# Performance work log

Hardware: AMD Instinct MI355X
Metric: run time of the kernel (lower is better)

## Reference

```python
import jax
import jax.numpy as jnp
from jax import lax
import numpy as np

EMBED_DIM = 768
NUM_HEADS = 12
BATCH = 8
SEQ = 1024
EPS = 1e-07
QK_QBIT = 8
QK_KBIT = 8
AV_ABIT = 8
AV_VBIT = 8
PROJ_WBIT = 8
PROJ_XBIT = 8
SCALE = EMBED_DIM ** (-0.5)  # module uses embed_dim, not head_dim


def _ste(hard, soft):
    # straight-through estimator: forward = hard, backward grad = d(soft)
    return soft + lax.stop_gradient(hard - soft)


def fake_quant_signed(x, bit):
    # _quantize_signed_matrix_train: sign/abs, global-max scaling, STE clamp + round
    sign = lax.stop_gradient(jnp.sign(x))
    a = jnp.abs(x)
    scaling = lax.stop_gradient(jnp.max(a)) + EPS
    y = a / scaling
    y = _ste(jnp.clip(y, 0.0, 1.0), y)          # Clamp.apply (STE)
    levels = 2.0 ** (bit - 1.0) - 1.0
    y = _ste(jnp.round(y * levels) / levels, y)  # Round.apply (STE)
    return y * scaling * sign


def fake_quant_unsigned(x, bit):
    # _quantize_unsigned_matrix_train
    scaling = lax.stop_gradient(jnp.max(x)) + EPS
    y = x / scaling
    y = _ste(jnp.clip(y, 0.0, 1.0), y)
    levels = 2.0 ** bit - 1.0
    y = _ste(jnp.round(y * levels) / levels, y)
    return y * scaling


def asim_linear(x, w, b, wbit, xbit):
    # ASiMLinear in 'Train' mode with signed_act=True: fake-quantize activation
    # and weight, dense matmul, trim_noise=0 -> no perturbation.
    xq = fake_quant_signed(x, xbit)
    wq = fake_quant_signed(w, wbit)
    return jnp.einsum('bnc,oc->bno', xq, wq) + b


def setup_inputs() -> dict:
    key = jax.random.key(0)
    k_x, k_qw, k_qb, k_pw, k_pb = jax.random.split(key, 5)
    x = jax.random.normal(k_x, (BATCH, SEQ, EMBED_DIM), dtype=jnp.float32)
    s = 1.0 / np.sqrt(EMBED_DIM)
    qkv_w = jax.random.normal(k_qw, (3 * EMBED_DIM, EMBED_DIM), dtype=jnp.float32) * s
    qkv_b = jax.random.normal(k_qb, (3 * EMBED_DIM,), dtype=jnp.float32) * 0.01
    proj_w = jax.random.normal(k_pw, (EMBED_DIM, EMBED_DIM), dtype=jnp.float32) * s
    proj_b = jax.random.normal(k_pb, (EMBED_DIM,), dtype=jnp.float32) * 0.01
    return {'x': x, 'qkv_w': qkv_w, 'qkv_b': qkv_b, 'proj_w': proj_w, 'proj_b': proj_b}


def reference(x, qkv_w, qkv_b, proj_w, proj_b):
    B, N, C = x.shape
    H = NUM_HEADS
    D = C // H
    # qkv projection (ASiMLinear, Train mode)
    qkv = asim_linear(x, qkv_w, qkv_b, PROJ_WBIT, PROJ_XBIT)      # [B, N, 3C]
    qkv = qkv.reshape(B, N, 3, H, D).transpose(2, 0, 3, 1, 4)      # [3, B, H, N, D]
    q, k, v = qkv[0], qkv[1], qkv[2]
    # _qk_train: fake-quantize q and k^T, matmul (trim_noise=0 -> no perturb)
    qq = fake_quant_signed(q, QK_QBIT)
    kq = fake_quant_signed(jnp.swapaxes(k, -2, -1), QK_KBIT)
    attn = jnp.einsum('bhnd,bhdm->bhnm', qq, kq) * SCALE           # [B, H, N, N]
    attn = jax.nn.softmax(attn, axis=-1)
    # dropout ratio 0.0 -> identity
    # _av_train: unsigned fake-quant of attention, signed fake-quant of v
    aq = fake_quant_unsigned(attn, AV_ABIT)
    vq = fake_quant_signed(v, AV_VBIT)
    out = jnp.einsum('bhnm,bhmd->bhnd', aq, vq)                    # [B, H, N, D]
    out = out.transpose(0, 2, 1, 3).reshape(B, N, C)
    # output projection (ASiMLinear, Train mode)
    out = asim_linear(out, proj_w, proj_b, PROJ_WBIT, PROJ_XBIT)
    return out
```

## Files before the change

kernel.cpp:

```cpp
#include <hip/hip_runtime.h>
#include <hip/hip_bf16.h>
#include <cstdint>
#include <cstddef>

#define B_    8
#define SEQ_  1024
#define C_    768
#define H_    12
#define D_    64
#define TC_   2304
#define M_    8192
#define EPS_  1e-7f
#define SCALE_ 0.036084391824351615f

typedef __attribute__((ext_vector_type(8))) short bf16x8;
typedef __attribute__((ext_vector_type(4))) float f32x4;
typedef __attribute__((ext_vector_type(4))) int   i32x4;

__device__ __forceinline__ bf16x8 expand8(int2 raw) {
  union { int2 v; signed char c[8]; } u; u.v = raw;
  bf16x8 r;
  #pragma unroll
  for (int j = 0; j < 8; ++j) {
    float f = (float)(int)u.c[j];
    r[j] = (short)(__float_as_uint(f) >> 16);
  }
  return r;
}
__device__ __forceinline__ void expand16(int4 raw, int4& lo, int4& hi) {
  union { int4 v; signed char c[16]; } u; u.v = raw;
  unsigned short s[16];
  #pragma unroll
  for (int j = 0; j < 16; ++j) {
    float f = (float)(int)u.c[j];
    s[j] = (unsigned short)(__float_as_uint(f) >> 16);
  }
  lo = *(const int4*)&s[0]; hi = *(const int4*)&s[8];
}

__device__ __forceinline__ int8_t quant1(float v, float s) {
  float y = fminf(fabsf(v) / s, 1.0f);
  int q = (int)rintf(y * 127.0f);
  return (int8_t)(v < 0.f ? -q : q);
}

__global__ void k_init(float* g) {
  if (threadIdx.x == 0) {
    g[0]=0.f; g[1]=0.f; g[2]=0.f; g[3]=0.f; g[4]=0.f; g[5]=0.f;
    g[6]=3.402823466e+38f;
    g[7]=0.f;
  }
}

__global__ __launch_bounds__(256) void k_absmax_fused(const float4* __restrict__ x,
                                                      const float4* __restrict__ w1,
                                                      const float4* __restrict__ w2,
                                                      float* g) {
  __shared__ float red[4];
  const int blk = blockIdx.x;
  const float4* p; unsigned n4; float* gout; int b0, nb;
  if (blk < 384)      { p = x;  n4 = 1572864u; gout = &g[0]; b0 = 0;   nb = 384; }
  else if (blk < 480) { p = w1; n4 = 442368u;  gout = &g[1]; b0 = 384; nb = 96;  }
  else                { p = w2; n4 = 147456u;  gout = &g[2]; b0 = 480; nb = 48;  }
  float m = 0.f;
  for (unsigned i = (unsigned)(blk - b0) * 256u + threadIdx.x; i < n4; i += (unsigned)nb * 256u) {
    float4 v = p[i];
    m = fmaxf(m, fmaxf(fmaxf(fabsf(v.x), fabsf(v.y)), fmaxf(fabsf(v.z), fabsf(v.w))));
  }
  #pragma unroll
  for (int off = 32; off; off >>= 1) m = fmaxf(m, __shfl_xor(m, off));
  if ((threadIdx.x & 63) == 0) red[threadIdx.x >> 6] = m;
  __syncthreads();
  if (threadIdx.x == 0) {
    m = fmaxf(fmaxf(red[0], red[1]), fmaxf(red[2], red[3]));
    atomicMax((unsigned int*)gout, __float_as_uint(m));
  }
}

__device__ __forceinline__ void quant_seg8(const float* __restrict__ in, unsigned n, float s,
                                           int8_t* __restrict__ out, unsigned i0, unsigned stride) {
  for (unsigned i = i0; i < n; i += stride)
    out[i] = quant1(in[i], s);
}
__global__ __launch_bounds__(256) void k_quant_fused(const float* __restrict__ x,
                                                     const float* __restrict__ w1,
                                                     const float* __restrict__ w2,
                                                     const float* __restrict__ g,
                                                     int8_t* __restrict__ xq,
                                                     int8_t* __restrict__ wq,
                                                     int8_t* __restrict__ pw) {
  const int blk = blockIdx.x;
  if (blk < 1536)      quant_seg8(x,  6291456u, g[0] + EPS_, xq, (unsigned)blk * 256u + threadIdx.x, 1536u * 256u);
  else if (blk < 1968) quant_seg8(w1, 1769472u, g[1] + EPS_, wq, (unsigned)(blk - 1536) * 256u + threadIdx.x, 432u * 256u);
  else                 quant_seg8(w2,  589824u, g[2] + EPS_, pw, (unsigned)(blk - 1968) * 256u + threadIdx.x, 144u * 256u);
}

__global__ __launch_bounds__(256) void k_quant_i8(const float* __restrict__ in, unsigned n,
                                                  const float* __restrict__ gmax,
                                                  int8_t* __restrict__ out) {
  const float s = *gmax + EPS_;
  quant_seg8(in, n, s, out, blockIdx.x * blockDim.x + threadIdx.x, gridDim.x * blockDim.x);
}

__global__ __launch_bounds__(256) void k_gemm8i(const int8_t* __restrict__ A,
                                                const int8_t* __restrict__ Bt,
                                                const float* __restrict__ bias,
                                                float* __restrict__ C,
                                                int Mn, int Nn, int Kn,
                                                const float* __restrict__ sA, const float* __restrict__ sB,
                                                float* pmax, int partDiv) {
  const int tid = threadIdx.x;
  int flat = blockIdx.y * gridDim.x + blockIdx.x;
  int chunk = (gridDim.x * gridDim.y) >> 3;
  int nf = (flat & 7) * chunk + (flat >> 3);
  const int n0 = (nf % gridDim.x) * 128, m0 = (nf / gridDim.x) * 128;
  const int wid = tid >> 6, lane = tid & 63;
  const int wr = wid >> 1, wc = wid & 1;
  const int lrow = lane & 15;
  const int lslot = lane >> 4;
  i32x4 acc[4][4] = {};
  const int8_t* pa = A  + (size_t)(m0 + wr * 64 + lrow) * Kn + lslot * 16;
  const int8_t* pb = Bt + (size_t)(n0 + wc * 64 + lrow) * Kn + lslot * 16;
  const size_t rs = (size_t)16 * Kn;
  #pragma unroll 4
  for (int k = 0; k < Kn; k += 64) {
    i32x4 af[4], bfr[4];
    #pragma unroll
    for (int i = 0; i < 4; ++i) af[i]  = *(const i32x4*)(pa + i * rs + k);
    #pragma unroll
    for (int j = 0; j < 4; ++j) bfr[j] = *(const i32x4*)(pb + j * rs + k);
    #pragma unroll
    for (int i = 0; i < 4; ++i)
      #pragma unroll
      for (int j = 0; j < 4; ++j)
        acc[i][j] = __builtin_amdgcn_mfma_i32_16x16x64_i8(af[i], bfr[j], acc[i][j], 0, 0, 0);
  }
  const float alpha = (sA[0] + EPS_) * (sB[0] + EPS_) * (1.0f / 16129.0f);
  const int orow = (lane >> 4) << 2;
  float amax = 0.f;
  #pragma unroll
  for (int i = 0; i < 4; ++i) {
    #pragma unroll
    for (int j = 0; j < 4; ++j) {
      int col = n0 + wc * 64 + j * 16 + lrow;
      float bc = bias[col];
      #pragma unroll
      for (int rr = 0; rr < 4; ++rr) {
        int row = m0 + wr * 64 + i * 16 + orow + rr;
        float val = (float)acc[i][j][rr] * alpha + bc;
        C[(size_t)row * Nn + col] = val;
        amax = fmaxf(amax, fabsf(val));
      }
    }
  }
  if (pmax) {
    #pragma unroll
    for (int off = 32; off; off >>= 1) amax = fmaxf(amax, __shfl_xor(amax, off));
    if (lane == 0) atomicMax((unsigned int*)&pmax[n0 / partDiv], __float_as_uint(amax));
  }
}

__global__ __launch_bounds__(256) void k_quant_heads(const float* __restrict__ qkvf, const float* __restrict__ g,
                                                     int8_t* __restrict__ qo, int8_t* __restrict__ ko,
                                                     int8_t* __restrict__ vT) {
  __shared__ float vt[64][65];
  const int bh = blockIdx.x >> 4, nt = blockIdx.x & 15;
  const int b = bh / 12, h = bh % 12;
  const int n0 = nt * 64;
  const int tid = threadIdx.x;
  const float s0 = g[3] + EPS_, s1 = g[4] + EPS_, s2 = g[5] + EPS_;
  const int r = tid >> 2, dc = tid & 3;
  const size_t mrow = (size_t)(b * 1024 + n0 + r) * 2304;
  union { int4 v; int8_t c[16]; } pk;
  {
    const float* src = qkvf + mrow + h * 64 + dc * 16;
    #pragma unroll
    for (int e = 0; e < 16; ++e) pk.c[e] = quant1(src[e], s0);
    *(int4*)&qo[((size_t)bh * 1024 + n0 + r) * 64 + dc * 16] = pk.v;
  }
  {
    const float* src = qkvf + mrow + 768 + h * 64 + dc * 16;
    #pragma unroll
    for (int e = 0; e < 16; ++e) pk.c[e] = quant1(src[e], s1);
    *(int4*)&ko[((size_t)bh * 1024 + n0 + r) * 64 + dc * 16] = pk.v;
  }
  {
    const float* src = qkvf + mrow + 1536 + h * 64 + dc * 16;
    #pragma unroll
    for (int e = 0; e < 16; ++e) vt[dc * 16 + e][r] = src[e];
  }
  __syncthreads();
  {
    const int d = tid >> 2, nc = tid & 3;
    #pragma unroll
    for (int e = 0; e < 16; ++e) pk.c[e] = quant1(vt[d][nc * 16 + e], s2);
    *(int4*)&vT[((size_t)bh * 64 + d) * 1024 + n0 + nc * 16] = pk.v;
  }
}

__global__ __launch_bounds__(256) void k_attn_stats_mfma(
    const int8_t* __restrict__ qi8, const int8_t* __restrict__ ki8,
    const float* __restrict__ g, float* __restrict__ rowmax, float* __restrict__ denomv,
    unsigned int* __restrict__ gminden) {
  __shared__ unsigned short Ks[64 * 64];
  __shared__ float red[4];
  const int bh = blockIdx.x >> 4, rt = blockIdx.x & 15;
  const int tid = threadIdx.x, w = tid >> 6, lane = tid & 63;
  const int lrow = lane & 15, lko = (lane >> 4) << 3;
  const int8_t* qbase = qi8 + (size_t)bh * 65536;
  const int8_t* kbase = ki8 + (size_t)bh * 65536;
  bf16x8 qf[2];
  #pragma unroll
  for (int ks = 0; ks < 2; ++ks)
    qf[ks] = expand8(*(const int2*)(qbase + (size_t)(rt*64 + w*16 + lrow) * 64 + ks*32 + lko));
  const float qkScale = (g[3] + EPS_) * (g[4] + EPS_) * (1.0f / 16129.0f) * SCALE_;
  float m = -3.0e38f, den = 0.f;
  const int srow = tid >> 2, sc = tid & 3;
  const int sx = (srow & 7) << 4;
  int4 kraw = *(const int4*)(kbase + (size_t)srow * 64 + sc * 16);
  for (int t = 0; t < 16; ++t) {
    __syncthreads();
    {
      int4 lo, hi; expand16(kraw, lo, hi);
      int bb = srow * 128 + sc * 32;
      *(int4*)((char*)Ks + ( bb       ^ sx)) = lo;
      *(int4*)((char*)Ks + ((bb + 16) ^ sx)) = hi;
    }
    if (t < 15)
      kraw = *(const int4*)(kbase + (size_t)(t + 1) * 4096 + (size_t)srow * 64 + sc * 16);
    __syncthreads();
    f32x4 acc[4] = {};
    #pragma unroll
    for (int ks = 0; ks < 2; ++ks)
      #pragma unroll
      for (int j = 0; j < 4; ++j) {
        int row = j * 16 + lrow;
        bf16x8 kf = *(const bf16x8*)((const char*)Ks + ((row * 128 + (ks*32 + lko) * 2) ^ ((row & 7) << 4)));
        acc[j] = __builtin_amdgcn_mfma_f32_16x16x32_bf16(kf, qf[ks], acc[j], 0, 0, 0);
      }
    float mnew = m;
    #pragma unroll
    for (int j = 0; j < 4; ++j)
      #pragma unroll
      for (int rr = 0; rr < 4; ++rr)
        mnew = fmaxf(mnew, acc[j][rr] * qkScale);
    float d = den * __expf(m - mnew);
    #pragma unroll
    for (int j = 0; j < 4; ++j)
      #pragma unroll
      for (int rr = 0; rr < 4; ++rr)
        d += __expf(acc[j][rr] * qkScale - mnew);
    den = d; m = mnew;
  }
  #pragma unroll
  for (int off = 16; off <= 32; off <<= 1) {
    float mo = __shfl_xor(m, off);
    float doo = __shfl_xor(den, off);
    float mg = fmaxf(m, mo);
    den = den * __expf(m - mg) + doo * __expf(mo - mg);
    m = mg;
  }
  if (lane < 16) {
    size_t rg = (size_t)bh * 1024 + rt * 64 + w * 16 + lane;
    rowmax[rg] = m;
    denomv[rg] = den;
  }
  float bm = den;
  #pragma unroll
  for (int off = 1; off < 16; off <<= 1) bm = fminf(bm, __shfl_xor(bm, off));
  if (lane == 0) red[w] = bm;
  __syncthreads();
  if (tid == 0)
    atomicMin(gminden, __float_as_uint(fminf(fminf(red[0], red[1]), fminf(red[2], red[3]))));
}

__global__ __launch_bounds__(256) void k_attn_pv_mfma(
    const int8_t* __restrict__ qi8, const int8_t* __restrict__ ki8, const int8_t* __restrict__ vti8,
    const float* __restrict__ g, const unsigned int* __restrict__ gminden,
    const float* __restrict__ rowmax, const float* __restrict__ denomv,
    float* __restrict__ aof, float* __restrict__ gamax) {
  __shared__ unsigned short Ks[64 * 64];
  __shared__ unsigned short Vs[64 * 64];
  __shared__ unsigned short Ps[64 * 64];
  __shared__ float red[4];
  const int bh = blockIdx.x >> 4, rt = blockIdx.x & 15;
  const int b = bh / 12, h = bh % 12;
  const int tid = threadIdx.x, w = tid >> 6, lane = tid & 63;
  const int lrow = lane & 15, lko = (lane >> 4) << 3;
  const int8_t* qbase = qi8 + (size_t)bh * 65536;
  const int8_t* kbase = ki8 + (size_t)bh * 65536;
  const int8_t* vbase = vti8 + (size_t)bh * 65536;
  bf16x8 qf[2];
  #pragma unroll
  for (int ks = 0; ks < 2; ++ks)
    qf[ks] = expand8(*(const int2*)(qbase + (size_t)(rt*64 + w*16 + lrow) * 64 + ks*32 + lko));
  const float qkScale = (g[3] + EPS_) * (g[4] + EPS_) * (1.0f / 16129.0f) * SCALE_;
  const float minden = __uint_as_float(*gminden);
  const float sa = 1.0f / minden + EPS_;
  const float invSa = 1.0f / sa;
  const float sv = g[5] + EPS_;
  const float pvScale = sa * sv * (1.0f / 32385.0f);
  const float rm  = rowmax[(size_t)bh * 1024 + rt * 64 + w * 16 + lrow];
  const float ivd = 1.0f / denomv[(size_t)bh * 1024 + rt * 64 + w * 16 + lrow];
  f32x4 accO[4] = {};
  const int srow = tid >> 2, sc = tid & 3;
  const int sx = (srow & 7) << 4;
  int4 kraw = *(const int4*)(kbase + (size_t)srow * 64 + sc * 16);
  int4 vraw = *(const int4*)(vbase + (size_t)srow * 1024 + sc * 16);
  for (int t = 0; t < 16; ++t) {
    __syncthreads();
    {
      int4 lo, hi;
      int bb = srow * 128 + sc * 32;
      expand16(kraw, lo, hi);
      *(int4*)((char*)Ks + ( bb       ^ sx)) = lo;
      *(int4*)((char*)Ks + ((bb + 16) ^ sx)) = hi;
      expand16(vraw, lo, hi);
      *(int4*)((char*)Vs + ( bb       ^ sx)) = lo;
      *(int4*)((char*)Vs + ((bb + 16) ^ sx)) = hi;
    }
    if (t < 15) {
      kraw = *(const int4*)(kbase + (size_t)(t + 1) * 4096 + (size_t)srow * 64 + sc * 16);
      vraw = *(const int4*)(vbase + (size_t)srow * 1024 + (t + 1) * 64 + sc * 16);
    }
    __syncthreads();
    f32x4 acc[4] = {};
    #pragma unroll
    for (int ks = 0; ks < 2; ++ks)
      #pragma unroll
      for (int j = 0; j < 4; ++j) {
        int row = j * 16 + lrow;
        bf16x8 kf = *(const bf16x8*)((const char*)Ks + ((row * 128 + (ks*32 + lko) * 2) ^ ((row & 7) << 4)));
        acc[j] = __builtin_amdgcn_mfma_f32_16x16x32_bf16(kf, qf[ks], acc[j], 0, 0, 0);
      }
    const int q = w * 16 + lrow;
    const int kb = (lane >> 4) << 2;
    #pragma unroll
    for (int j = 0; j < 4; ++j) {
      float a0 = rintf(fminf(__expf(acc[j][0] * qkScale - rm) * ivd * invSa, 1.0f) * 255.0f);
      float a1 = rintf(fminf(__expf(acc[j][1] * qkScale - rm) * ivd * invSa, 1.0f) * 255.0f);
      float a2 = rintf(fminf(__expf(acc[j][2] * qkScale - rm) * ivd * invSa, 1.0f) * 255.0f);
      float a3 = rintf(fminf(__expf(acc[j][3] * qkScale - rm) * ivd * invSa, 1.0f) * 255.0f);
      uint2 pk;
      pk.x = (__float_as_uint(a0) >> 16) | ((__float_as_uint(a1) >> 16) << 16);
      pk.y = (__float_as_uint(a2) >> 16) | ((__float_as_uint(a3) >> 16) << 16);
      int byteoff = (q * 128 + (j * 16 + kb) * 2) ^ ((q & 7) << 4);
      *(uint2*)((char*)Ps + byteoff) = pk;
    }
    #pragma unroll
    for (int ks = 0; ks < 2; ++ks) {
      bf16x8 pf = *(const bf16x8*)((const char*)Ps + ((q * 128 + (ks*32 + lko) * 2) ^ ((q & 7) << 4)));
      #pragma unroll
      for (int j = 0; j < 4; ++j) {
        int row = j * 16 + lrow;
        bf16x8 vf = *(const bf16x8*)((const char*)Vs + ((row * 128 + (ks*32 + lko) * 2) ^ ((row & 7) << 4)));
        accO[j] = __builtin_amdgcn_mfma_f32_16x16x32_bf16(pf, vf, accO[j], 0, 0, 0);
      }
    }
  }
  float amax = 0.f;
  #pragma unroll
  for (int j = 0; j < 4; ++j) {
    int d = j * 16 + lrow;
    #pragma unroll
    for (int rr = 0; rr < 4; ++rr) {
      int row = rt * 64 + w * 16 + (lane >> 4) * 4 + rr;
      float val = accO[j][rr] * pvScale;
      aof[((size_t)(b * 1024 + row)) * 768 + h * 64 + d] = val;
      amax = fmaxf(amax, fabsf(val));
    }
  }
  #pragma unroll
  for (int off = 1; off < 64; off <<= 1) amax = fmaxf(amax, __shfl_xor(amax, off));
  if (lane == 0) red[w] = amax;
  __syncthreads();
  if (tid == 0)
    atomicMax((unsigned int*)gamax, __float_as_uint(fmaxf(fmaxf(red[0], red[1]), fmaxf(red[2], red[3]))));
}

extern "C" void kernel_launch(void* const* d_in, const int* in_sizes, int n_in,
                              void* d_out, int out_size, void* d_ws, size_t ws_size,
                              hipStream_t stream) {
  const float* x      = (const float*)d_in[0];
  const float* qkv_w  = (const float*)d_in[1];
  const float* qkv_b  = (const float*)d_in[2];
  const float* proj_w = (const float*)d_in[3];
  const float* proj_b = (const float*)d_in[4];
  float* out = (float*)d_out;

  char* w = (char*)d_ws;
  float*          g      = (float*)(w + 0);
  float*          rowmax = (float*)(w + 256);
  float*          denomv = (float*)(w + 393472);
  int8_t*         qi8    = (int8_t*)(w + 786688);
  int8_t*         ki8    = (int8_t*)(w + 7078144);
  int8_t*         vT     = (int8_t*)(w + 13369600);
  int8_t*         pw8    = (int8_t*)(w + 19661056);
  int8_t*         xq8    = (int8_t*)(w + 20840704);
  int8_t*         wq8    = (int8_t*)(w + 33423616);
  float*          qkvf   = (float*)(w + 36962560);
  float*          aof    = (float*)(w + 36962560);
  int8_t*         aob8   = (int8_t*)(w + 62128384);

  hipLaunchKernelGGL(k_init, dim3(1), dim3(64), 0, stream, g);

  hipLaunchKernelGGL(k_absmax_fused, dim3(528), dim3(256), 0, stream,
                     (const float4*)x, (const float4*)qkv_w, (const float4*)proj_w, g);

  hipLaunchKernelGGL(k_quant_fused, dim3(2112), dim3(256), 0, stream,
                     x, qkv_w, proj_w, g, xq8, wq8, pw8);

  hipLaunchKernelGGL(k_gemm8i, dim3(TC_ / 128, M_ / 128), dim3(256), 0, stream,
                     xq8, wq8, qkv_b, qkvf, M_, TC_, C_, &g[0], &g[1], &g[3], 768);

  hipLaunchKernelGGL(k_quant_heads, dim3(1536), dim3(256), 0, stream, qkvf, g, qi8, ki8, vT);

  hipLaunchKernelGGL(k_attn_stats_mfma, dim3(1536), dim3(256), 0, stream,
                     qi8, ki8, g, rowmax, denomv, (unsigned int*)&g[6]);
  hipLaunchKernelGGL(k_attn_pv_mfma, dim3(1536), dim3(256), 0, stream,
                     qi8, ki8, vT, g, (const unsigned int*)&g[6], rowmax, denomv, aof, &g[7]);

  hipLaunchKernelGGL(k_quant_i8, dim3(2048), dim3(256), 0, stream, aof, 6291456u, &g[7], aob8);

  hipLaunchKernelGGL(k_gemm8i, dim3(C_ / 128, M_ / 128), dim3(256), 0, stream,
                     aob8, pw8, proj_b, out, M_, C_, C_, &g[7], &g[2], (float*)nullptr, 1);

  (void)in_sizes; (void)n_in; (void)out_size; (void)ws_size;
}
```

Measured before the change: 258.4 us.

## Stage int8 GEMM tiles through LDS with register-prefetched double buffering

The int8 GEMM now loads each 128x64 A and B tile from global memory once per block into shared memory, instead of each wave reading its own fragments directly from global. Global loads for the next two K steps are prefetched into registers while the current tile is consumed from LDS. This is meant to cut redundant global and L2 traffic and hide load latency. In exchange it adds two barriers per K step and more register pressure. Any K that is not a multiple of 128 would need care, but the shapes used here (768) divide evenly.

After: 236.3 us. -8.6%, faster.

```diff
diff --git a/kernel.cpp b/kernel.cpp
--- a/kernel.cpp
+++ b/kernel.cpp
@@ -109,6 +109,8 @@
                                                 int Mn, int Nn, int Kn,
                                                 const float* __restrict__ sA, const float* __restrict__ sB,
                                                 float* pmax, int partDiv) {
+  __shared__ int8_t As[4][128][16];
+  __shared__ int8_t Bs[4][128][16];
   const int tid = threadIdx.x;
   int flat = blockIdx.y * gridDim.x + blockIdx.x;
   int chunk = (gridDim.x * gridDim.y) >> 3;
@@ -119,22 +121,50 @@
   const int lrow = lane & 15;
   const int lslot = lane >> 4;
   i32x4 acc[4][4] = {};
-  const int8_t* pa = A  + (size_t)(m0 + wr * 64 + lrow) * Kn + lslot * 16;
-  const int8_t* pb = Bt + (size_t)(n0 + wc * 64 + lrow) * Kn + lslot * 16;
-  const size_t rs = (size_t)16 * Kn;
-  #pragma unroll 4
-  for (int k = 0; k < Kn; k += 64) {
-    i32x4 af[4], bfr[4];
-    #pragma unroll
-    for (int i = 0; i < 4; ++i) af[i]  = *(const i32x4*)(pa + i * rs + k);
-    #pragma unroll
-    for (int j = 0; j < 4; ++j) bfr[j] = *(const i32x4*)(pb + j * rs + k);
-    #pragma unroll
-    for (int i = 0; i < 4; ++i)
-      #pragma unroll
-      for (int j = 0; j < 4; ++j)
-        acc[i][j] = __builtin_amdgcn_mfma_i32_16x16x64_i8(af[i], bfr[j], acc[i][j], 0, 0, 0);
-  }
+  const int srow = tid & 127;
+  const int slot0 = tid >> 7;
+  const int8_t* ga = A  + (size_t)(m0 + srow) * Kn + slot0 * 16;
+  const int8_t* gb = Bt + (size_t)(n0 + srow) * Kn + slot0 * 16;
+  const int nt = Kn >> 6;
+  int4 ra0_0 = *(const int4*)(ga);
+  int4 ra1_0 = *(const int4*)(ga + 32);
+  int4 rb0_0 = *(const int4*)(gb);
+  int4 rb1_0 = *(const int4*)(gb + 32);
+  int4 ra0_1 = *(const int4*)(ga + 64);
+  int4 ra1_1 = *(const int4*)(ga + 96);
+  int4 rb0_1 = *(const int4*)(gb + 64);
+  int4 rb1_1 = *(const int4*)(gb + 96);
+  #define KSTEP(SET, T)                                                        \
+    if (T) __syncthreads();                                                    \
+    *(int4*)&As[slot0][srow][0]     = ra0_##SET;                               \
+    *(int4*)&As[slot0 + 2][srow][0] = ra1_##SET;                               \
+    *(int4*)&Bs[slot0][srow][0]     = rb0_##SET;                               \
+    *(int4*)&Bs[slot0 + 2][srow][0] = rb1_##SET;                               \
+    if ((T) + 2 < nt) {                                                        \
+      const int ko_ = ((T) + 2) << 6;                                          \
+      ra0_##SET = *(const int4*)(ga + ko_);                                    \
+      ra1_##SET = *(const int4*)(ga + ko_ + 32);                               \
+      rb0_##SET = *(const int4*)(gb + ko_);                                    \
+      rb1_##SET = *(const int4*)(gb + ko_ + 32);                               \
+    }                                                                          \
+    __syncthreads();                                                           \
+    {                                                                          \
+      i32x4 af[4], bfr[4];                                                     \
+      _Pragma("unroll")                                                        \
+      for (int i = 0; i < 4; ++i) af[i]  = *(const i32x4*)&As[lslot][wr * 64 + i * 16 + lrow][0]; \
+      _Pragma("unroll")                                                        \
+      for (int j = 0; j < 4; ++j) bfr[j] = *(const i32x4*)&Bs[lslot][wc * 64 + j * 16 + lrow][0]; \
+      _Pragma("unroll")                                                        \
+      for (int i = 0; i < 4; ++i)                                              \
+        _Pragma("unroll")                                                      \
+        for (int j = 0; j < 4; ++j)                                            \
+          acc[i][j] = __builtin_amdgcn_mfma_i32_16x16x64_i8(af[i], bfr[j], acc[i][j], 0, 0, 0); \
+    }
+  for (int t = 0; t < nt; t += 2) {
+    KSTEP(0, t)
+    KSTEP(1, t + 1)
+  }
+  #undef KSTEP
   const float alpha = (sA[0] + EPS_) * (sB[0] + EPS_) * (1.0f / 16129.0f);
   const int orow = (lane >> 4) << 2;
   float amax = 0.f;
```
